# Optimization experiments

Measured on AMD Instinct MI355X. Metric: run time of the kernel, lower is better.

The kernel has to match this reference:

```python
import jax, jax.numpy as jnp
import numpy as np
import math

B, S, D, H = 8, 256, 4096, 16
HD = D // H  # 256 == S, so the module's transposed mask application is exactly elementwise


def setup_inputs() -> dict:
    key = jax.random.key(0)
    ks = jax.random.split(key, 12)
    sc = 1.0 / math.sqrt(D)
    inp = {
        "q": jax.random.normal(ks[0], (B, S, D), dtype=jnp.float32),
        "k": jax.random.normal(ks[1], (B, S, D), dtype=jnp.float32),
        "v": jax.random.normal(ks[2], (B, S, D), dtype=jnp.float32),
        "mask": jax.random.randint(ks[3], (B, S), 0, 2),
        "Wq": jax.random.normal(ks[4], (D, D), dtype=jnp.float32) * sc,
        "bq": jnp.zeros((D,), dtype=jnp.float32),
        "Wk": jax.random.normal(ks[5], (D, D), dtype=jnp.float32) * sc,
        "bk": jnp.zeros((D,), dtype=jnp.float32),
        "Wv": jax.random.normal(ks[6], (D, D), dtype=jnp.float32) * sc,
        "bv": jnp.zeros((D,), dtype=jnp.float32),
        "Wo": jax.random.normal(ks[7], (D, D), dtype=jnp.float32) * sc,
        "bo": jnp.zeros((D,), dtype=jnp.float32),
    }
    return inp


def reference(q, k, v, mask, Wq, bq, Wk, bk, Wv, bv, Wo, bo):
    def proj(x, W, b):
        # nn.Linear: x @ W.T + b ; then [B,S,H,HD] -> [B,H,S,HD]
        return (x @ W.T + b).reshape(B, S, H, HD).transpose(0, 2, 1, 3)

    qh = proj(q, Wq, bq)
    kh = proj(k, Wk, bk)
    vh = proj(v, Wv, bv)

    # torch: attn_mask = (mask==0).view(bs,1,1,-1).repeat(1,H,HD,1) -> [B,H,HD,S]
    # then where(attn_mask, 0, q) against q of shape [B,H,S,HD] (elementwise since HD==S)
    am = jnp.broadcast_to((mask == 0)[:, None, None, :], (B, H, HD, S))
    qh = jnp.where(am, 0.0, qh)
    kh = jnp.where(am, 0.0, kh)

    scale = 1.0 / math.sqrt(HD)
    scores = jnp.einsum('bhqd,bhkd->bhqk', qh, kh) * scale
    w = jax.nn.softmax(scores, axis=-1)
    out = jnp.einsum('bhqk,bhkd->bhqd', w, vh)
    out = out.transpose(0, 2, 1, 3).reshape(B, S, D)
    out = out * (D ** -0.5)
    return out @ Wo.T + bo
```

## Files before the change

kernel.cpp:

```cpp
#include <hip/hip_runtime.h>


typedef _Float16 f16;
typedef f16 f16x8 __attribute__((ext_vector_type(8)));
typedef float f32x4 __attribute__((ext_vector_type(4)));

__device__ __forceinline__ void g2lds(const f16* g, f16* l) {
  __builtin_amdgcn_global_load_lds((const __attribute__((address_space(1))) void*)g,
                                   (__attribute__((address_space(3))) void*)l, 16, 0, 0);
}

__device__ __forceinline__ void cvt8(const float* src, f16* dst, int i) {
  float4 a = *(const float4*)(src + i);
  float4 b = *(const float4*)(src + i + 4);
  f16x8 o;
  o[0] = (f16)a.x; o[1] = (f16)a.y; o[2] = (f16)a.z; o[3] = (f16)a.w;
  o[4] = (f16)b.x; o[5] = (f16)b.y; o[6] = (f16)b.z; o[7] = (f16)b.w;
  *(f16x8*)(dst + i) = o;
}

__global__ __launch_bounds__(256) void cvt_x(const float* __restrict__ q,
                                             const float* __restrict__ k,
                                             const float* __restrict__ v,
                                             f16* __restrict__ oq, f16* __restrict__ ok,
                                             f16* __restrict__ ov) {
  const float* src; f16* dst;
  if (blockIdx.y == 0)      { src = q; dst = oq; }
  else if (blockIdx.y == 1) { src = k; dst = ok; }
  else                      { src = v; dst = ov; }
  cvt8(src, dst, (blockIdx.x * 256 + threadIdx.x) * 8);
}

__global__ __launch_bounds__(256) void cvt_w(const float* __restrict__ a,
                                             const float* __restrict__ b,
                                             const float* __restrict__ c,
                                             const float* __restrict__ d,
                                             f16* __restrict__ oa, f16* __restrict__ ob,
                                             f16* __restrict__ oc, f16* __restrict__ od) {
  const float* src; f16* dst;
  if (blockIdx.y == 0)      { src = a; dst = oa; }
  else if (blockIdx.y == 1) { src = b; dst = ob; }
  else if (blockIdx.y == 2) { src = c; dst = oc; }
  else                      { src = d; dst = od; }
  cvt8(src, dst, (blockIdx.x * 256 + threadIdx.x) * 8);
}

#define MFMA8x(ACC, FA, FB, MO, NO)                                             \
  do {                                                                          \
    __builtin_amdgcn_s_setprio(1);                                              \
    _Pragma("unroll")                                                           \
    for (int m_ = 0; m_ < (MO); ++m_)                                           \
      _Pragma("unroll")                                                         \
      for (int n_ = 0; n_ < (NO); ++n_)                                         \
        _Pragma("unroll")                                                       \
        for (int ks_ = 0; ks_ < 2; ++ks_)                                       \
          ACC = __builtin_amdgcn_mfma_f32_16x16x32_f16(FA[m_][ks_], FB[n_][ks_],\
                                                       ACC, 0, 0, 0);           \
    __builtin_amdgcn_s_setprio(0);                                              \
  } while (0)

__global__ __launch_bounds__(512, 2) void gemm256(
    const f16* __restrict__ Aq, const f16* __restrict__ Ak,
    const f16* __restrict__ Bq, const f16* __restrict__ Bk,
    const float* __restrict__ bq, const float* __restrict__ bk,
    const int* __restrict__ mask,
    f16* __restrict__ Qbh, f16* __restrict__ Kbh)
{
  __shared__ __align__(16) f16 lds[2][4][8192];
  const int tid = threadIdx.x;
  const int lane = tid & 63, wid = tid >> 6;
  const int wm = wid >> 2, wn = wid & 3;
  const int ln = lane & 15, lh = lane >> 4;
  const int lnx = ln & 7;
  const int K = 4096, NT = 64;

  const int seg = blockIdx.x >> 7;
  int inner = blockIdx.x & 127;
  inner = (inner & 7) * 16 + (inner >> 3);

  const f16* A   = (seg == 0) ? Aq : Ak;
  const f16* B   = (seg == 0) ? Bq : Bk;
  const float* bias = (seg == 0) ? bq : bk;
  const int bm = inner % 8, bn = inner / 8;

  const size_t Abase = (size_t)bm * 256 * K;
  const size_t Bbase = (size_t)bn * 256 * K;
  const int sr = tid >> 3;
  const int ss = (tid & 7) ^ (sr & 7);

#define STAGEC(tt, bb_, c)                                                       \
  do {                                                                           \
    const f16* base_ = ((c) < 2) ? A + Abase + (size_t)((c) * 128) * K           \
                                 : B + Bbase + (size_t)(((c) - 2) * 128) * K;    \
    f16* dst_ = &lds[bb_][c][0];                                                 \
    g2lds(base_ + (size_t)sr * K + ((tt) << 6) + ss * 8, dst_ + tid * 8);        \
    g2lds(base_ + (size_t)(64 + sr) * K + ((tt) << 6) + ss * 8,                  \
          dst_ + (512 + tid) * 8);                                               \
  } while (0)

#define RD_A03(buf) do { _Pragma("unroll")                                       \
  for (int m_ = 0; m_ < 4; ++m_) _Pragma("unroll")                               \
    for (int k_ = 0; k_ < 2; ++k_)                                               \
      a03[m_][k_] = *(const f16x8*)&(buf)[(m_ * 16 + ln) * 64 + ((k_ * 4 + lh) ^ lnx) * 8]; } while (0)
#define RD_A47(buf) do { _Pragma("unroll")                                       \
  for (int m_ = 0; m_ < 4; ++m_) _Pragma("unroll")                               \
    for (int k_ = 0; k_ < 2; ++k_)                                               \
      a47[m_][k_] = *(const f16x8*)&(buf)[((64 + m_ * 16) + ln) * 64 + ((k_ * 4 + lh) ^ lnx) * 8]; } while (0)
#define RD_B01(buf) do { _Pragma("unroll")                                       \
  for (int n_ = 0; n_ < 2; ++n_) _Pragma("unroll")                               \
    for (int k_ = 0; k_ < 2; ++k_)                                               \
      b01[n_][k_] = *(const f16x8*)&(buf)[(brow + n_ * 16 + ln) * 64 + ((k_ * 4 + lh) ^ lnx) * 8]; } while (0)
#define RD_B23(buf) do { _Pragma("unroll")                                       \
  for (int n_ = 0; n_ < 2; ++n_) _Pragma("unroll")                               \
    for (int k_ = 0; k_ < 2; ++k_)                                               \
      b23[n_][k_] = *(const f16x8*)&(buf)[(brow + 32 + n_ * 16 + ln) * 64 + ((k_ * 4 + lh) ^ lnx) * 8]; } while (0)

  f32x4 acc[8][4] = {};
  f16x8 a03[4][2], a47[4][2], b01[2][2], b23[2][2];
  const int brow = (wn & 1) * 64;

  STAGEC(0, 0, 0); STAGEC(0, 0, 1); STAGEC(0, 0, 2); STAGEC(0, 0, 3);
  STAGEC(1, 1, 0);
  asm volatile("s_waitcnt vmcnt(2)" ::: "memory");
  __builtin_amdgcn_s_barrier();
  {
    const f16* cA0 = &lds[0][wm][0];
    const f16* cB0 = &lds[0][2 + (wn >> 1)][0];
    RD_A03(cA0); RD_B01(cB0);
  }

  for (int t = 0; t < NT; ++t) {
    const int bb = t & 1;
    const f16* cA = &lds[bb][wm][0];
    const f16* cB = &lds[bb][2 + (wn >> 1)][0];
    const f16* cAn = &lds[bb ^ 1][wm][0];
    const f16* cBn = &lds[bb ^ 1][2 + (wn >> 1)][0];

    if (t + 1 < NT) { STAGEC(t + 1, bb ^ 1, 1); STAGEC(t + 1, bb ^ 1, 2); STAGEC(t + 1, bb ^ 1, 3); }
    RD_B23(cB);
    __builtin_amdgcn_s_barrier();
    MFMA8x(acc[m_][n_], a03, b01, 4, 2);

    RD_A47(cA);
    __builtin_amdgcn_s_barrier();
    MFMA8x(acc[m_][2 + n_], a03, b23, 4, 2);

    __builtin_amdgcn_s_barrier();
    MFMA8x(acc[4 + m_][n_], a47, b01, 4, 2);

    if (t + 2 < NT) {
      STAGEC(t + 2, bb, 0);
      asm volatile("s_waitcnt vmcnt(2)" ::: "memory");
    } else {
      asm volatile("s_waitcnt vmcnt(0)" ::: "memory");
    }
    asm volatile("s_waitcnt lgkmcnt(0)" ::: "memory");
    __builtin_amdgcn_s_barrier();
    if (t + 1 < NT) { RD_A03(cAn); RD_B01(cBn); }
    MFMA8x(acc[4 + m_][2 + n_], a47, b23, 4, 2);
  }
#undef STAGEC
#undef RD_A03
#undef RD_A47
#undef RD_B01
#undef RD_B23

#pragma unroll
  for (int mf = 0; mf < 8; ++mf)
#pragma unroll
    for (int nf = 0; nf < 4; ++nf)
#pragma unroll
      for (int i = 0; i < 4; ++i) {
        int R = bm * 256 + wm * 128 + mf * 16 + lh * 4 + i;
        int C = bn * 256 + wn * 64 + nf * 16 + ln;
        float v = acc[mf][nf][i];
        v += bias[C];
        v = mask[(R >> 8) * 256 + (C & 255)] ? v : 0.0f;
        f16* o = (seg == 0) ? Qbh : Kbh;
        o[(size_t)((R >> 8) * 16 + (C >> 8)) * 65536 +
          (size_t)(R & 255) * 256 + (C & 255)] = (f16)v;
      }
}

template<int EPI>
__global__ __launch_bounds__(512, 2) void gemm128(
    const f16* __restrict__ A, const f16* __restrict__ B,
    const float* __restrict__ bias, void* __restrict__ out,
    int M, int N, int K)
{
  __shared__ __align__(16) f16 lds[2 * 24576];
  const int tid = threadIdx.x;
  const int lane = tid & 63, wid = tid >> 6;
  const int wm = wid >> 2, wn = wid & 3;
  const int ln = lane & 15, lh = lane >> 4;
  const int lnx = ln & 7;
  const int bm = blockIdx.y, bn = blockIdx.x;

  const size_t Abase = (size_t)bm * 128 * K;
  const size_t Bbase = (size_t)bn * 256 * K;
  const int sr = tid >> 3;
  const int ss = (tid & 7) ^ (sr & 7);
  const int NT = K >> 6;

  f16* buf0 = &lds[0];
  f16* buf1 = &lds[24576];

#define STG1(t_, bo_)                                                           \
  do {                                                                          \
    const int kt_ = (t_) << 6;                                                  \
    g2lds(A + Abase + (size_t)sr * K + kt_ + ss * 8,         (bo_) + tid * 8);  \
    g2lds(A + Abase + (size_t)(64 + sr) * K + kt_ + ss * 8,  (bo_) + (512 + tid) * 8); \
  } while (0)
#define STG2(t_, bo_)                                                           \
  do {                                                                          \
    const int kt_ = (t_) << 6;                                                  \
    g2lds(B + Bbase + (size_t)sr * K + kt_ + ss * 8,         (bo_) + 8192 + tid * 8); \
    g2lds(B + Bbase + (size_t)(64 + sr) * K + kt_ + ss * 8,  (bo_) + 8192 + (512 + tid) * 8); \
    g2lds(B + Bbase + (size_t)(128 + sr) * K + kt_ + ss * 8, (bo_) + 8192 + (1024 + tid) * 8); \
    g2lds(B + Bbase + (size_t)(192 + sr) * K + kt_ + ss * 8, (bo_) + 8192 + (1536 + tid) * 8); \
  } while (0)

#define RD_A(fa, buf, mo) do { _Pragma("unroll")                                 \
  for (int m_ = 0; m_ < 2; ++m_) _Pragma("unroll")                               \
    for (int k_ = 0; k_ < 2; ++k_)                                               \
      fa[m_][k_] = *(const f16x8*)&(buf)[(wm * 64 + ((mo) + m_) * 16 + ln) * 64 + ((k_ * 4 + lh) ^ lnx) * 8]; } while (0)
#define RD_B(fb, buf, no) do { _Pragma("unroll")                                 \
  for (int n_ = 0; n_ < 2; ++n_) _Pragma("unroll")                               \
    for (int k_ = 0; k_ < 2; ++k_)                                               \
      fb[n_][k_] = *(const f16x8*)&(buf)[8192 + (wn * 64 + ((no) + n_) * 16 + ln) * 64 + ((k_ * 4 + lh) ^ lnx) * 8]; } while (0)

  f32x4 acc[4][4] = {};
  f16x8 a01[2][2], a23[2][2], b01[2][2], b23[2][2];

  STG1(0, buf0); STG2(0, buf0);
  STG1(1, buf1);
  asm volatile("s_waitcnt vmcnt(2)" ::: "memory");
  __builtin_amdgcn_s_barrier();
  RD_A(a01, buf0, 0); RD_B(b01, buf0, 0);

  for (int t = 0; t < NT; ++t) {
    f16* bb  = (t & 1) ? buf1 : buf0;
    f16* bbn = (t & 1) ? buf0 : buf1;

    if (t + 1 < NT) STG2(t + 1, bbn);
    RD_B(b23, bb, 2);
    __builtin_amdgcn_s_barrier();
    MFMA8x(acc[m_][n_], a01, b01, 2, 2);

    RD_A(a23, bb, 2);
    __builtin_amdgcn_s_barrier();
    MFMA8x(acc[m_][2 + n_], a01, b23, 2, 2);

    __builtin_amdgcn_s_barrier();
    MFMA8x(acc[2 + m_][n_], a23, b01, 2, 2);

    if (t + 2 < NT) {
      STG1(t + 2, bb);
      asm volatile("s_waitcnt vmcnt(2)" ::: "memory");
    } else {
      asm volatile("s_waitcnt vmcnt(0)" ::: "memory");
    }
    asm volatile("s_waitcnt lgkmcnt(0)" ::: "memory");
    __builtin_amdgcn_s_barrier();
    if (t + 1 < NT) { RD_A(a01, bbn, 0); RD_B(b01, bbn, 0); }
    MFMA8x(acc[2 + m_][2 + n_], a23, b23, 2, 2);
  }
#undef STG1
#undef STG2
#undef RD_A
#undef RD_B

#pragma unroll
  for (int mf = 0; mf < 4; ++mf)
#pragma unroll
    for (int nf = 0; nf < 4; ++nf)
#pragma unroll
      for (int i = 0; i < 4; ++i) {
        int R = bm * 128 + wm * 64 + mf * 16 + lh * 4 + i;
        int C = bn * 256 + wn * 64 + nf * 16 + ln;
        float v = acc[mf][nf][i];
        if (EPI == 1) {
          v += bias[R];
          ((f16*)out)[(size_t)(C >> 8) * 1048576 + (size_t)R * 256 + (C & 255)] = (f16)v;
        } else {
          v += bias[C];
          ((float*)out)[(size_t)R * N + C] = v;
        }
      }
}

__global__ __launch_bounds__(256) void attn_kernel(
    const f16* __restrict__ Q, const f16* __restrict__ Kt,
    const f16* __restrict__ Vt, f16* __restrict__ aout)
{
  __shared__ __align__(16) f16 tile[64 * 256];
  __shared__ __align__(16) f16 pbuf[64 * 256];
  const int tid = threadIdx.x;
  const int lane = tid & 63, w = tid >> 6;
  const int ln = lane & 15, lh = lane >> 4;
  const int bh = blockIdx.x >> 2, rb = blockIdx.x & 3;
  const int b = bh >> 4, h = bh & 15;
  const size_t hb = (size_t)bh * 65536;

  const int strow = tid >> 5;
  const int stsl  = (tid & 31) ^ (strow & 7);

  f16x8 aq[8];
  {
    const f16* qp = Q + hb + (size_t)(rb * 64 + w * 16 + ln) * 256;
#pragma unroll
    for (int ks = 0; ks < 8; ++ks)
      aq[ks] = *(const f16x8*)(qp + ks * 32 + lh * 8);
  }

  f32x4 sacc[16] = {};

  for (int kt = 0; kt < 4; ++kt) {
#pragma unroll
    for (int c = 0; c < 8; ++c) {
      int L = c * 256 + tid;
      int row = c * 8 + strow;
      g2lds(Kt + hb + (size_t)(kt * 64 + row) * 256 + stsl * 8, &tile[L * 8]);
    }
    __syncthreads();
#pragma unroll
    for (int nf = 0; nf < 4; ++nf) {
      f16x8 bf[8];
#pragma unroll
      for (int ks = 0; ks < 8; ++ks) {
        int r = nf * 16 + ln;
        int sl = (ks * 4 + lh) ^ (r & 7);
        bf[ks] = *(const f16x8*)&tile[r * 256 + sl * 8];
      }
#pragma unroll
      for (int ks = 0; ks < 8; ++ks)
        sacc[kt * 4 + nf] = __builtin_amdgcn_mfma_f32_16x16x32_f16(
            aq[ks], bf[ks], sacc[kt * 4 + nf], 0, 0, 0);
    }
    __syncthreads();
  }

  const float SC = 1.0f / 16.0f;
  float mrow[4] = {-1e30f, -1e30f, -1e30f, -1e30f};
#pragma unroll
  for (int t = 0; t < 16; ++t)
#pragma unroll
    for (int i = 0; i < 4; ++i) mrow[i] = fmaxf(mrow[i], sacc[t][i]);
#pragma unroll
  for (int i = 0; i < 4; ++i) {
    mrow[i] = fmaxf(mrow[i], __shfl_xor(mrow[i], 1));
    mrow[i] = fmaxf(mrow[i], __shfl_xor(mrow[i], 2));
    mrow[i] = fmaxf(mrow[i], __shfl_xor(mrow[i], 4));
    mrow[i] = fmaxf(mrow[i], __shfl_xor(mrow[i], 8));
  }
  float ssum[4] = {0.f, 0.f, 0.f, 0.f};
#pragma unroll
  for (int t = 0; t < 16; ++t)
#pragma unroll
    for (int i = 0; i < 4; ++i) {
      float p = __expf((sacc[t][i] - mrow[i]) * SC);
      sacc[t][i] = p;
      ssum[i] += p;
    }
#pragma unroll
  for (int i = 0; i < 4; ++i) {
    ssum[i] += __shfl_xor(ssum[i], 1);
    ssum[i] += __shfl_xor(ssum[i], 2);
    ssum[i] += __shfl_xor(ssum[i], 4);
    ssum[i] += __shfl_xor(ssum[i], 8);
  }
  float rs[4];
#pragma unroll
  for (int i = 0; i < 4; ++i) rs[i] = 1.0f / ssum[i];

#pragma unroll
  for (int t = 0; t < 16; ++t)
#pragma unroll
    for (int i = 0; i < 4; ++i) {
      int row = w * 16 + lh * 4 + i;
      int col = (t >> 2) * 64 + (t & 3) * 16 + ln;
      pbuf[row * 256 + (col ^ ((row & 7) << 3))] = (f16)(sacc[t][i] * rs[i]);
    }

  f16x8 pa[8];
  {
    int r = w * 16 + ln;
#pragma unroll
    for (int ks = 0; ks < 8; ++ks) {
      int col = ks * 32 + lh * 8;
      pa[ks] = *(const f16x8*)&pbuf[r * 256 + (col ^ ((r & 7) << 3))];
    }
  }

  for (int dt = 0; dt < 4; ++dt) {
#pragma unroll
    for (int c = 0; c < 8; ++c) {
      int L = c * 256 + tid;
      int row = c * 8 + strow;
      g2lds(Vt + hb + (size_t)(dt * 64 + row) * 256 + stsl * 8, &tile[L * 8]);
    }
    __syncthreads();
    f32x4 oacc[4] = {};
#pragma unroll
    for (int nf = 0; nf < 4; ++nf) {
      f16x8 bf[8];
#pragma unroll
      for (int ks = 0; ks < 8; ++ks) {
        int r = nf * 16 + ln;
        int sl = (ks * 4 + lh) ^ (r & 7);
        bf[ks] = *(const f16x8*)&tile[r * 256 + sl * 8];
      }
#pragma unroll
      for (int ks = 0; ks < 8; ++ks)
        oacc[nf] = __builtin_amdgcn_mfma_f32_16x16x32_f16(pa[ks], bf[ks], oacc[nf], 0, 0, 0);
    }
#pragma unroll
    for (int nf = 0; nf < 4; ++nf)
#pragma unroll
      for (int i = 0; i < 4; ++i) {
        int s = rb * 64 + w * 16 + lh * 4 + i;
        int d = dt * 64 + nf * 16 + ln;
        aout[(size_t)(b * 256 + s) * 4096 + h * 256 + d] = (f16)(oacc[nf][i] * 0.015625f);
      }
    __syncthreads();
  }
}

extern "C" void kernel_launch(void* const* d_in, const int* in_sizes, int n_in,
                              void* d_out, int out_size, void* d_ws, size_t ws_size,
                              hipStream_t stream) {
  const float* q  = (const float*)d_in[0];
  const float* k  = (const float*)d_in[1];
  const float* v  = (const float*)d_in[2];
  const int*   mk = (const int*)d_in[3];
  const float* Wq = (const float*)d_in[4];
  const float* bq = (const float*)d_in[5];
  const float* Wk = (const float*)d_in[6];
  const float* bk = (const float*)d_in[7];
  const float* Wv = (const float*)d_in[8];
  const float* bv = (const float*)d_in[9];
  const float* Wo = (const float*)d_in[10];
  const float* bo = (const float*)d_in[11];
  float* out = (float*)d_out;

  const size_t NQ = 2048ull * 4096;
  const size_t NW = 4096ull * 4096;
  f16* ws = (f16*)d_ws;
  f16* q16  = ws;
  f16* k16  = q16 + NQ;
  f16* v16  = k16 + NQ;
  f16* Wq16 = v16 + NQ;
  f16* Wk16 = Wq16 + NW;
  f16* Wv16 = Wk16 + NW;
  f16* Wo16 = Wv16 + NW;
  f16* Qbh  = Wo16 + NW;
  f16* Kbh  = Qbh + NQ;
  f16* Vt   = Kbh + NQ;
  f16* at16 = Vt + NQ;

  cvt_x<<<dim3(4096, 3), 256, 0, stream>>>(q, k, v, q16, k16, v16);
  cvt_w<<<dim3(8192, 4), 256, 0, stream>>>(Wq, Wk, Wv, Wo, Wq16, Wk16, Wv16, Wo16);

  gemm256<<<256, 512, 0, stream>>>(q16, k16, Wq16, Wk16, bq, bk, mk, Qbh, Kbh);
  gemm128<1><<<dim3(8, 32), 512, 0, stream>>>(Wv16, v16, bv, Vt, 4096, 2048, 4096);
  attn_kernel<<<512, 256, 0, stream>>>(Qbh, Kbh, Vt, at16);
  gemm128<2><<<dim3(16, 16), 512, 0, stream>>>(at16, Wo16, bo, out, 2048, 4096, 4096);
}
```

Baseline: 394.2 us.

## Fuse Wq/Wk fp32-to-fp16 conversion into projection GEMM and triple-buffer gemm128

```diff
diff --git a/kernel.cpp b/kernel.cpp
--- a/kernel.cpp
+++ b/kernel.cpp
@@ -31,17 +31,12 @@
   cvt8(src, dst, (blockIdx.x * 256 + threadIdx.x) * 8);
 }
 
-__global__ __launch_bounds__(256) void cvt_w(const float* __restrict__ a,
-                                             const float* __restrict__ b,
-                                             const float* __restrict__ c,
-                                             const float* __restrict__ d,
-                                             f16* __restrict__ oa, f16* __restrict__ ob,
-                                             f16* __restrict__ oc, f16* __restrict__ od) {
+__global__ __launch_bounds__(256) void cvt_w2(const float* __restrict__ a,
+                                              const float* __restrict__ b,
+                                              f16* __restrict__ oa, f16* __restrict__ ob) {
   const float* src; f16* dst;
-  if (blockIdx.y == 0)      { src = a; dst = oa; }
-  else if (blockIdx.y == 1) { src = b; dst = ob; }
-  else if (blockIdx.y == 2) { src = c; dst = oc; }
-  else                      { src = d; dst = od; }
+  if (blockIdx.y == 0) { src = a; dst = oa; }
+  else                 { src = b; dst = ob; }
   cvt8(src, dst, (blockIdx.x * 256 + threadIdx.x) * 8);
 }
 
@@ -61,7 +56,7 @@
 
 __global__ __launch_bounds__(512, 2) void gemm256(
     const f16* __restrict__ Aq, const f16* __restrict__ Ak,
-    const f16* __restrict__ Bq, const f16* __restrict__ Bk,
+    const float* __restrict__ Bq, const float* __restrict__ Bk,
     const float* __restrict__ bq, const float* __restrict__ bk,
     const int* __restrict__ mask,
     f16* __restrict__ Qbh, f16* __restrict__ Kbh)
@@ -78,24 +73,58 @@
   int inner = blockIdx.x & 127;
   inner = (inner & 7) * 16 + (inner >> 3);
 
-  const f16* A   = (seg == 0) ? Aq : Ak;
-  const f16* B   = (seg == 0) ? Bq : Bk;
+  const f16* A     = (seg == 0) ? Aq : Ak;
+  const float* B   = (seg == 0) ? Bq : Bk;
   const float* bias = (seg == 0) ? bq : bk;
   const int bm = inner % 8, bn = inner / 8;
 
   const size_t Abase = (size_t)bm * 256 * K;
   const size_t Bbase = (size_t)bn * 256 * K;
+
   const int sr = tid >> 3;
   const int ss = (tid & 7) ^ (sr & 7);
-
-#define STAGEC(tt, bb_, c)                                                       \
+  const int br = tid >> 2;
+  const int bj = tid & 3;
+  const int bs0 = ((bj * 2) ^ (br & 7)) * 8;
+  const int bs1 = ((bj * 2 + 1) ^ (br & 7)) * 8;
+
+#define STAGE_A(tt, bb_)                                                         \
   do {                                                                           \
-    const f16* base_ = ((c) < 2) ? A + Abase + (size_t)((c) * 128) * K           \
-                                 : B + Bbase + (size_t)(((c) - 2) * 128) * K;    \
-    f16* dst_ = &lds[bb_][c][0];                                                 \
-    g2lds(base_ + (size_t)sr * K + ((tt) << 6) + ss * 8, dst_ + tid * 8);        \
-    g2lds(base_ + (size_t)(64 + sr) * K + ((tt) << 6) + ss * 8,                  \
-          dst_ + (512 + tid) * 8);                                               \
+    const int kt_ = (tt) << 6;                                                   \
+    g2lds(A + Abase + (size_t)sr * K + kt_ + ss * 8,        &lds[bb_][0][0] + tid * 8); \
+    g2lds(A + Abase + (size_t)(64 + sr) * K + kt_ + ss * 8, &lds[bb_][0][0] + (512 + tid) * 8); \
+    g2lds(A + Abase + (size_t)(128 + sr) * K + kt_ + ss * 8, &lds[bb_][1][0] + tid * 8); \
+    g2lds(A + Abase + (size_t)(192 + sr) * K + kt_ + ss * 8, &lds[bb_][1][0] + (512 + tid) * 8); \
+  } while (0)
+
+  float4 rb0, rb1, rb2, rb3, rb4, rb5, rb6, rb7;
+
+#define BLOAD(tt)                                                                \
+  do {                                                                           \
+    const int kt_ = (tt) << 6;                                                   \
+    const float* p0_ = B + Bbase + (size_t)br * K + kt_ + bj * 16;               \
+    const float* p1_ = B + Bbase + (size_t)(128 + br) * K + kt_ + bj * 16;       \
+    rb0 = *(const float4*)(p0_);      rb1 = *(const float4*)(p0_ + 4);           \
+    rb2 = *(const float4*)(p0_ + 8);  rb3 = *(const float4*)(p0_ + 12);          \
+    rb4 = *(const float4*)(p1_);      rb5 = *(const float4*)(p1_ + 4);           \
+    rb6 = *(const float4*)(p1_ + 8);  rb7 = *(const float4*)(p1_ + 12);          \
+  } while (0)
+
+#define PACK8(w_, xa_, xb_)                                                      \
+  do {                                                                           \
+    w_[0] = (f16)xa_.x; w_[1] = (f16)xa_.y; w_[2] = (f16)xa_.z; w_[3] = (f16)xa_.w; \
+    w_[4] = (f16)xb_.x; w_[5] = (f16)xb_.y; w_[6] = (f16)xb_.z; w_[7] = (f16)xb_.w; \
+  } while (0)
+
+#define BWRITE(bb_)                                                              \
+  do {                                                                           \
+    f16x8 w0_, w1_, w2_, w3_;                                                    \
+    PACK8(w0_, rb0, rb1); PACK8(w1_, rb2, rb3);                                  \
+    PACK8(w2_, rb4, rb5); PACK8(w3_, rb6, rb7);                                  \
+    *(f16x8*)(&lds[bb_][2][0] + br * 64 + bs0) = w0_;                            \
+    *(f16x8*)(&lds[bb_][2][0] + br * 64 + bs1) = w1_;                            \
+    *(f16x8*)(&lds[bb_][3][0] + br * 64 + bs0) = w2_;                            \
+    *(f16x8*)(&lds[bb_][3][0] + br * 64 + bs1) = w3_;                            \
   } while (0)
 
 #define RD_A03(buf) do { _Pragma("unroll")                                       \
@@ -119,9 +148,10 @@
   f16x8 a03[4][2], a47[4][2], b01[2][2], b23[2][2];
   const int brow = (wn & 1) * 64;
 
-  STAGEC(0, 0, 0); STAGEC(0, 0, 1); STAGEC(0, 0, 2); STAGEC(0, 0, 3);
-  STAGEC(1, 1, 0);
-  asm volatile("s_waitcnt vmcnt(2)" ::: "memory");
+  STAGE_A(0, 0); BLOAD(0);
+  asm volatile("s_waitcnt vmcnt(0)" ::: "memory");
+  BWRITE(0);
+  asm volatile("s_waitcnt lgkmcnt(0)" ::: "memory");
   __builtin_amdgcn_s_barrier();
   {
     const f16* cA0 = &lds[0][wm][0];
@@ -132,11 +162,11 @@
   for (int t = 0; t < NT; ++t) {
     const int bb = t & 1;
     const f16* cA = &lds[bb][wm][0];
+    const f16* cAn = &lds[bb ^ 1][wm][0];
     const f16* cB = &lds[bb][2 + (wn >> 1)][0];
-    const f16* cAn = &lds[bb ^ 1][wm][0];
     const f16* cBn = &lds[bb ^ 1][2 + (wn >> 1)][0];
 
-    if (t + 1 < NT) { STAGEC(t + 1, bb ^ 1, 1); STAGEC(t + 1, bb ^ 1, 2); STAGEC(t + 1, bb ^ 1, 3); }
+    if (t + 1 < NT) { STAGE_A(t + 1, bb ^ 1); BLOAD(t + 1); }
     RD_B23(cB);
     __builtin_amdgcn_s_barrier();
     MFMA8x(acc[m_][n_], a03, b01, 4, 2);
@@ -148,18 +178,19 @@
     __builtin_amdgcn_s_barrier();
     MFMA8x(acc[4 + m_][n_], a47, b01, 4, 2);
 
-    if (t + 2 < NT) {
-      STAGEC(t + 2, bb, 0);
-      asm volatile("s_waitcnt vmcnt(2)" ::: "memory");
-    } else {
+    if (t + 1 < NT) {
       asm volatile("s_waitcnt vmcnt(0)" ::: "memory");
+      BWRITE(bb ^ 1);
     }
     asm volatile("s_waitcnt lgkmcnt(0)" ::: "memory");
     __builtin_amdgcn_s_barrier();
     if (t + 1 < NT) { RD_A03(cAn); RD_B01(cBn); }
     MFMA8x(acc[4 + m_][2 + n_], a47, b23, 4, 2);
   }
-#undef STAGEC
+#undef STAGE_A
+#undef BLOAD
+#undef PACK8
+#undef BWRITE
 #undef RD_A03
 #undef RD_A47
 #undef RD_B01
@@ -183,17 +214,16 @@
 }
 
 template<int EPI>
-__global__ __launch_bounds__(512, 2) void gemm128(
+__global__ __launch_bounds__(512, 2) void gemm_dp(
     const f16* __restrict__ A, const f16* __restrict__ B,
     const float* __restrict__ bias, void* __restrict__ out,
     int M, int N, int K)
 {
-  __shared__ __align__(16) f16 lds[2 * 24576];
+  __shared__ __align__(16) f16 lds[3 * 24576];
   const int tid = threadIdx.x;
   const int lane = tid & 63, wid = tid >> 6;
   const int wm = wid >> 2, wn = wid & 3;
   const int ln = lane & 15, lh = lane >> 4;
-  const int lnx = ln & 7;
   const int bm = blockIdx.y, bn = blockIdx.x;
 
   const size_t Abase = (size_t)bm * 128 * K;
@@ -202,73 +232,89 @@
   const int ss = (tid & 7) ^ (sr & 7);
   const int NT = K >> 6;
 
-  f16* buf0 = &lds[0];
-  f16* buf1 = &lds[24576];
-
-#define STG1(t_, bo_)                                                           \
+  f16* p0 = &lds[0];
+  f16* p1 = &lds[24576];
+  f16* p2 = &lds[2 * 24576];
+
+#define STAGE(t_, bo_, part)                                                    \
   do {                                                                          \
     const int kt_ = (t_) << 6;                                                  \
-    g2lds(A + Abase + (size_t)sr * K + kt_ + ss * 8,         (bo_) + tid * 8);  \
-    g2lds(A + Abase + (size_t)(64 + sr) * K + kt_ + ss * 8,  (bo_) + (512 + tid) * 8); \
-  } while (0)
-#define STG2(t_, bo_)                                                           \
+    if ((part) == 0) {                                                          \
+      g2lds(A + Abase + (size_t)sr * K + kt_ + ss * 8,         (bo_) + tid * 8);  \
+      g2lds(B + Bbase + (size_t)sr * K + kt_ + ss * 8,         (bo_) + 8192 + tid * 8); \
+      g2lds(B + Bbase + (size_t)(64 + sr) * K + kt_ + ss * 8,  (bo_) + 8192 + (512 + tid) * 8); \
+    } else {                                                                    \
+      g2lds(A + Abase + (size_t)(64 + sr) * K + kt_ + ss * 8,  (bo_) + (512 + tid) * 8); \
+      g2lds(B + Bbase + (size_t)(128 + sr) * K + kt_ + ss * 8, (bo_) + 8192 + (1024 + tid) * 8); \
+      g2lds(B + Bbase + (size_t)(192 + sr) * K + kt_ + ss * 8, (bo_) + 8192 + (1536 + tid) * 8); \
+    }                                                                           \
+  } while (0)
+
+  const int lx = ln & 7;
+  const int arow = (wm * 64 + ln) * 64;
+  const int brow = (wn * 64 + ln) * 64;
+
+#define LOADFRAGS(fa, fb, buf, ks)                                              \
   do {                                                                          \
-    const int kt_ = (t_) << 6;                                                  \
-    g2lds(B + Bbase + (size_t)sr * K + kt_ + ss * 8,         (bo_) + 8192 + tid * 8); \
-    g2lds(B + Bbase + (size_t)(64 + sr) * K + kt_ + ss * 8,  (bo_) + 8192 + (512 + tid) * 8); \
-    g2lds(B + Bbase + (size_t)(128 + sr) * K + kt_ + ss * 8, (bo_) + 8192 + (1024 + tid) * 8); \
-    g2lds(B + Bbase + (size_t)(192 + sr) * K + kt_ + ss * 8, (bo_) + 8192 + (1536 + tid) * 8); \
-  } while (0)
-
-#define RD_A(fa, buf, mo) do { _Pragma("unroll")                                 \
-  for (int m_ = 0; m_ < 2; ++m_) _Pragma("unroll")                               \
-    for (int k_ = 0; k_ < 2; ++k_)                                               \
-      fa[m_][k_] = *(const f16x8*)&(buf)[(wm * 64 + ((mo) + m_) * 16 + ln) * 64 + ((k_ * 4 + lh) ^ lnx) * 8]; } while (0)
-#define RD_B(fb, buf, no) do { _Pragma("unroll")                                 \
-  for (int n_ = 0; n_ < 2; ++n_) _Pragma("unroll")                               \
-    for (int k_ = 0; k_ < 2; ++k_)                                               \
-      fb[n_][k_] = *(const f16x8*)&(buf)[8192 + (wn * 64 + ((no) + n_) * 16 + ln) * 64 + ((k_ * 4 + lh) ^ lnx) * 8]; } while (0)
+    const f16* bA_ = (buf);                                                     \
+    const f16* bB_ = (buf) + 8192;                                              \
+    const int so_ = (((ks) * 4 + lh) ^ lx) * 8;                                 \
+    _Pragma("unroll")                                                           \
+    for (int mf = 0; mf < 4; ++mf)                                              \
+      fa[mf] = *(const f16x8*)&bA_[arow + mf * 1024 + so_];                     \
+    _Pragma("unroll")                                                           \
+    for (int nf = 0; nf < 4; ++nf)                                              \
+      fb[nf] = *(const f16x8*)&bB_[brow + nf * 1024 + so_];                     \
+  } while (0)
+
+#define MFMA16(fa, fb)                                                          \
+  do {                                                                          \
+    __builtin_amdgcn_s_setprio(1);                                              \
+    _Pragma("unroll")                                                           \
+    for (int mf = 0; mf < 4; ++mf)                                              \
+      _Pragma("unroll")                                                         \
+      for (int nf = 0; nf < 4; ++nf)                                            \
+        acc[mf][nf] = __builtin_amdgcn_mfma_f32_16x16x32_f16(fa[mf], fb[nf],    \
+                                                             acc[mf][nf], 0, 0, 0); \
+    __builtin_amdgcn_s_setprio(0);                                              \
+  } while (0)
 
   f32x4 acc[4][4] = {};
-  f16x8 a01[2][2], a23[2][2], b01[2][2], b23[2][2];
-
-  STG1(0, buf0); STG2(0, buf0);
-  STG1(1, buf1);
-  asm volatile("s_waitcnt vmcnt(2)" ::: "memory");
+  f16x8 ca[4], cb[4], na[4], nb[4];
+
+  STAGE(0, p0, 0); STAGE(0, p0, 1);
+  STAGE(1, p1, 0); STAGE(1, p1, 1);
+  asm volatile("s_waitcnt vmcnt(6)" ::: "memory");
   __builtin_amdgcn_s_barrier();
-  RD_A(a01, buf0, 0); RD_B(b01, buf0, 0);
+  asm volatile("" ::: "memory");
+  LOADFRAGS(ca, cb, p0, 0);
 
   for (int t = 0; t < NT; ++t) {
-    f16* bb  = (t & 1) ? buf1 : buf0;
-    f16* bbn = (t & 1) ? buf0 : buf1;
-
-    if (t + 1 < NT) STG2(t + 1, bbn);
-    RD_B(b23, bb, 2);
-    __builtin_amdgcn_s_barrier();
-    MFMA8x(acc[m_][n_], a01, b01, 2, 2);
-
-    RD_A(a23, bb, 2);
-    __builtin_amdgcn_s_barrier();
-    MFMA8x(acc[m_][2 + n_], a01, b23, 2, 2);
-
-    __builtin_amdgcn_s_barrier();
-    MFMA8x(acc[2 + m_][n_], a23, b01, 2, 2);
-
-    if (t + 2 < NT) {
-      STG1(t + 2, bb);
-      asm volatile("s_waitcnt vmcnt(2)" ::: "memory");
+    LOADFRAGS(na, nb, p0, 1);
+    if (t + 2 < NT) { STAGE(t + 2, p2, 0); STAGE(t + 2, p2, 1); }
+    MFMA16(ca, cb);
+
+    if (t + 1 < NT) {
+      if (t + 2 < NT) {
+        asm volatile("s_waitcnt vmcnt(6)" ::: "memory");
+      } else {
+        asm volatile("s_waitcnt vmcnt(0)" ::: "memory");
+      }
+      __builtin_amdgcn_s_barrier();
+      asm volatile("" ::: "memory");
+      LOADFRAGS(ca, cb, p1, 0);
+      MFMA16(na, nb);
+      asm volatile("" ::: "memory");
+      __builtin_amdgcn_s_barrier();
+      asm volatile("" ::: "memory");
+      f16* tp = p0; p0 = p1; p1 = p2; p2 = tp;
     } else {
-      asm volatile("s_waitcnt vmcnt(0)" ::: "memory");
-    }
-    asm volatile("s_waitcnt lgkmcnt(0)" ::: "memory");
-    __builtin_amdgcn_s_barrier();
-    if (t + 1 < NT) { RD_A(a01, bbn, 0); RD_B(b01, bbn, 0); }
-    MFMA8x(acc[2 + m_][2 + n_], a23, b23, 2, 2);
-  }
-#undef STG1
-#undef STG2
-#undef RD_A
-#undef RD_B
+      MFMA16(na, nb);
+    }
+  }
+#undef STAGE
+#undef LOADFRAGS
+#undef MFMA16
 
 #pragma unroll
   for (int mf = 0; mf < 4; ++mf)
@@ -459,10 +505,10 @@
   f16* at16 = Vt + NQ;
 
   cvt_x<<<dim3(4096, 3), 256, 0, stream>>>(q, k, v, q16, k16, v16);
-  cvt_w<<<dim3(8192, 4), 256, 0, stream>>>(Wq, Wk, Wv, Wo, Wq16, Wk16, Wv16, Wo16);
-
-  gemm256<<<256, 512, 0, stream>>>(q16, k16, Wq16, Wk16, bq, bk, mk, Qbh, Kbh);
-  gemm128<1><<<dim3(8, 32), 512, 0, stream>>>(Wv16, v16, bv, Vt, 4096, 2048, 4096);
+  cvt_w2<<<dim3(8192, 2), 256, 0, stream>>>(Wv, Wo, Wv16, Wo16);
+
+  gemm256<<<256, 512, 0, stream>>>(q16, k16, Wq, Wk, bq, bk, mk, Qbh, Kbh);
+  gemm_dp<1><<<dim3(8, 32), 512, 0, stream>>>(Wv16, v16, bv, Vt, 4096, 2048, 4096);
   attn_kernel<<<512, 256, 0, stream>>>(Qbh, Kbh, Vt, at16);
-  gemm128<2><<<dim3(16, 16), 512, 0, stream>>>(at16, Wo16, bo, out, 2048, 4096, 4096);
-}
+  gemm_dp<2><<<dim3(16, 16), 512, 0, stream>>>(at16, Wo16, bo, out, 2048, 4096, 4096);
+}
```

New measurement: 419.5 us. 6.4% more time.

## Replace pipelined 128x256 GEMM with simpler 128x128 single-buffer GEMM kernel

Applied to the files above, without the earlier changes.

```diff
diff --git a/kernel.cpp b/kernel.cpp
--- a/kernel.cpp
+++ b/kernel.cpp
@@ -183,92 +183,59 @@
 }
 
 template<int EPI>
-__global__ __launch_bounds__(512, 2) void gemm128(
+__global__ __launch_bounds__(256) void gemm97(
     const f16* __restrict__ A, const f16* __restrict__ B,
-    const float* __restrict__ bias, void* __restrict__ out,
-    int M, int N, int K)
+    const float* __restrict__ bias, void* __restrict__ out, int N, int K)
 {
-  __shared__ __align__(16) f16 lds[2 * 24576];
+  __shared__ __align__(16) f16 lA[128 * 64];
+  __shared__ __align__(16) f16 lB[128 * 64];
   const int tid = threadIdx.x;
   const int lane = tid & 63, wid = tid >> 6;
-  const int wm = wid >> 2, wn = wid & 3;
+  const int wm = wid >> 1, wn = wid & 1;
   const int ln = lane & 15, lh = lane >> 4;
-  const int lnx = ln & 7;
-  const int bm = blockIdx.y, bn = blockIdx.x;
+  const int lx = ln & 7;
+  const int bm = blockIdx.x, bn = blockIdx.y;
 
   const size_t Abase = (size_t)bm * 128 * K;
-  const size_t Bbase = (size_t)bn * 256 * K;
+  const size_t Bbase = (size_t)bn * 128 * K;
   const int sr = tid >> 3;
   const int ss = (tid & 7) ^ (sr & 7);
   const int NT = K >> 6;
 
-  f16* buf0 = &lds[0];
-  f16* buf1 = &lds[24576];
-
-#define STG1(t_, bo_)                                                           \
-  do {                                                                          \
-    const int kt_ = (t_) << 6;                                                  \
-    g2lds(A + Abase + (size_t)sr * K + kt_ + ss * 8,         (bo_) + tid * 8);  \
-    g2lds(A + Abase + (size_t)(64 + sr) * K + kt_ + ss * 8,  (bo_) + (512 + tid) * 8); \
-  } while (0)
-#define STG2(t_, bo_)                                                           \
-  do {                                                                          \
-    const int kt_ = (t_) << 6;                                                  \
-    g2lds(B + Bbase + (size_t)sr * K + kt_ + ss * 8,         (bo_) + 8192 + tid * 8); \
-    g2lds(B + Bbase + (size_t)(64 + sr) * K + kt_ + ss * 8,  (bo_) + 8192 + (512 + tid) * 8); \
-    g2lds(B + Bbase + (size_t)(128 + sr) * K + kt_ + ss * 8, (bo_) + 8192 + (1024 + tid) * 8); \
-    g2lds(B + Bbase + (size_t)(192 + sr) * K + kt_ + ss * 8, (bo_) + 8192 + (1536 + tid) * 8); \
-  } while (0)
-
-#define RD_A(fa, buf, mo) do { _Pragma("unroll")                                 \
-  for (int m_ = 0; m_ < 2; ++m_) _Pragma("unroll")                               \
-    for (int k_ = 0; k_ < 2; ++k_)                                               \
-      fa[m_][k_] = *(const f16x8*)&(buf)[(wm * 64 + ((mo) + m_) * 16 + ln) * 64 + ((k_ * 4 + lh) ^ lnx) * 8]; } while (0)
-#define RD_B(fb, buf, no) do { _Pragma("unroll")                                 \
-  for (int n_ = 0; n_ < 2; ++n_) _Pragma("unroll")                               \
-    for (int k_ = 0; k_ < 2; ++k_)                                               \
-      fb[n_][k_] = *(const f16x8*)&(buf)[8192 + (wn * 64 + ((no) + n_) * 16 + ln) * 64 + ((k_ * 4 + lh) ^ lnx) * 8]; } while (0)
+  const int arow = (wm * 64 + ln) * 64;
+  const int brow = (wn * 64 + ln) * 64;
 
   f32x4 acc[4][4] = {};
-  f16x8 a01[2][2], a23[2][2], b01[2][2], b23[2][2];
-
-  STG1(0, buf0); STG2(0, buf0);
-  STG1(1, buf1);
-  asm volatile("s_waitcnt vmcnt(2)" ::: "memory");
-  __builtin_amdgcn_s_barrier();
-  RD_A(a01, buf0, 0); RD_B(b01, buf0, 0);
 
   for (int t = 0; t < NT; ++t) {
-    f16* bb  = (t & 1) ? buf1 : buf0;
-    f16* bbn = (t & 1) ? buf0 : buf1;
-
-    if (t + 1 < NT) STG2(t + 1, bbn);
-    RD_B(b23, bb, 2);
-    __builtin_amdgcn_s_barrier();
-    MFMA8x(acc[m_][n_], a01, b01, 2, 2);
-
-    RD_A(a23, bb, 2);
-    __builtin_amdgcn_s_barrier();
-    MFMA8x(acc[m_][2 + n_], a01, b23, 2, 2);
-
-    __builtin_amdgcn_s_barrier();
-    MFMA8x(acc[2 + m_][n_], a23, b01, 2, 2);
-
-    if (t + 2 < NT) {
-      STG1(t + 2, bb);
-      asm volatile("s_waitcnt vmcnt(2)" ::: "memory");
-    } else {
-      asm volatile("s_waitcnt vmcnt(0)" ::: "memory");
-    }
-    asm volatile("s_waitcnt lgkmcnt(0)" ::: "memory");
-    __builtin_amdgcn_s_barrier();
-    if (t + 1 < NT) { RD_A(a01, bbn, 0); RD_B(b01, bbn, 0); }
-    MFMA8x(acc[2 + m_][2 + n_], a23, b23, 2, 2);
-  }
-#undef STG1
-#undef STG2
-#undef RD_A
-#undef RD_B
+    const int kt = t << 6;
+#pragma unroll
+    for (int j = 0; j < 4; ++j) {
+      g2lds(A + Abase + (size_t)(j * 32 + sr) * K + kt + ss * 8, lA + j * 2048 + tid * 8);
+      g2lds(B + Bbase + (size_t)(j * 32 + sr) * K + kt + ss * 8, lB + j * 2048 + tid * 8);
+    }
+    __syncthreads();
+    f16x8 af[4][2], bf[4][2];
+#pragma unroll
+    for (int mf = 0; mf < 4; ++mf)
+#pragma unroll
+      for (int ks = 0; ks < 2; ++ks)
+        af[mf][ks] = *(const f16x8*)&lA[arow + mf * 1024 + ((ks * 4 + lh) ^ lx) * 8];
+#pragma unroll
+    for (int nf = 0; nf < 4; ++nf)
+#pragma unroll
+      for (int ks = 0; ks < 2; ++ks)
+        bf[nf][ks] = *(const f16x8*)&lB[brow + nf * 1024 + ((ks * 4 + lh) ^ lx) * 8];
+#pragma unroll
+    for (int mf = 0; mf < 4; ++mf)
+#pragma unroll
+      for (int nf = 0; nf < 4; ++nf)
+#pragma unroll
+        for (int ks = 0; ks < 2; ++ks)
+          acc[mf][nf] = __builtin_amdgcn_mfma_f32_16x16x32_f16(
+              af[mf][ks], bf[nf][ks], acc[mf][nf], 0, 0, 0);
+    __syncthreads();
+  }
 
 #pragma unroll
   for (int mf = 0; mf < 4; ++mf)
@@ -277,7 +244,7 @@
 #pragma unroll
       for (int i = 0; i < 4; ++i) {
         int R = bm * 128 + wm * 64 + mf * 16 + lh * 4 + i;
-        int C = bn * 256 + wn * 64 + nf * 16 + ln;
+        int C = bn * 128 + wn * 64 + nf * 16 + ln;
         float v = acc[mf][nf][i];
         if (EPI == 1) {
           v += bias[R];
@@ -462,7 +429,7 @@
   cvt_w<<<dim3(8192, 4), 256, 0, stream>>>(Wq, Wk, Wv, Wo, Wq16, Wk16, Wv16, Wo16);
 
   gemm256<<<256, 512, 0, stream>>>(q16, k16, Wq16, Wk16, bq, bk, mk, Qbh, Kbh);
-  gemm128<1><<<dim3(8, 32), 512, 0, stream>>>(Wv16, v16, bv, Vt, 4096, 2048, 4096);
+  gemm97<1><<<dim3(32, 16), 256, 0, stream>>>(Wv16, v16, bv, Vt, 2048, 4096);
   attn_kernel<<<512, 256, 0, stream>>>(Qbh, Kbh, Vt, at16);
-  gemm128<2><<<dim3(16, 16), 512, 0, stream>>>(at16, Wo16, bo, out, 2048, 4096, 4096);
-}
+  gemm97<2><<<dim3(16, 32), 256, 0, stream>>>(at16, Wo16, bo, out, 4096, 4096);
+}
```

After: 424.9 us. 1.08x slower.
